# Optimization experiments

Hardware: AMD Instinct MI355X
Metric: run time of the kernel (lower is better)

## Reference

```python
import jax, jax.numpy as jnp
import numpy as np

B, TU, TZ, V, H, E = 64, 128, 16, 32000, 512, 256
EPS = 1e-10


def setup_inputs() -> dict:
    key = jax.random.key(0)
    ks = jax.random.split(key, 22)
    s = 0.02  # weight init scale
    inp = {
        "embed_z": jax.random.normal(ks[0], (1, B, E), jnp.float32),
        "last_hidden": jax.random.normal(ks[1], (1, B, H), jnp.float32),
        "u_enc_out": jax.random.normal(ks[2], (TU, B, H), jnp.float32),
        # previous-turn z posterior: rows are probability distributions over vocab
        "pv_pz_proba": jax.nn.softmax(jax.random.normal(ks[3], (TZ, B, V), jnp.float32), axis=-1),
        "pv_z_dec_out": jax.random.normal(ks[4], (TZ, B, H), jnp.float32),
        "rand_eps": jax.random.normal(ks[5], (B, E), jnp.float32),
        "u_input_np": jax.random.randint(ks[6], (TU, B), 0, V),
        "u_input": jax.random.randint(ks[6], (TU, B), 0, V),   # unused by forward
        "m_input_np": jax.random.randint(ks[7], (TU, B), 0, V),  # unused by forward
        # GRU (single layer, single step)
        "W_ih": jax.random.normal(ks[8], (3 * H, E), jnp.float32) * s,
        "W_hh": jax.random.normal(ks[9], (3 * H, H), jnp.float32) * s,
        "b_ih": jnp.zeros((3 * H,), jnp.float32),
        "b_hh": jnp.zeros((3 * H,), jnp.float32),
        # w1: hidden -> vocab
        "W_w1": jax.random.normal(ks[10], (V, H), jnp.float32) * s,
        "b_w1": jnp.zeros((V,), jnp.float32),
        # proj_copy1 / proj_copy2: hidden -> hidden
        "W_p1": jax.random.normal(ks[11], (H, H), jnp.float32) * s,
        "b_p1": jnp.zeros((H,), jnp.float32),
        "W_p2": jax.random.normal(ks[12], (H, H), jnp.float32) * s,
        "b_p2": jnp.zeros((H,), jnp.float32),
        # mu / log_sigma: vocab -> embed
        "W_mu": jax.random.normal(ks[13], (E, V), jnp.float32) * s,
        "b_mu": jnp.zeros((E,), jnp.float32),
        "W_ls": jax.random.normal(ks[14], (E, V), jnp.float32) * s,
        "b_ls": jnp.zeros((E,), jnp.float32),
    }
    return inp


def reference(embed_z, last_hidden, u_enc_out, pv_pz_proba, pv_z_dec_out, rand_eps,
              u_input_np, u_input, m_input_np,
              W_ih, W_hh, b_ih, b_hh, W_w1, b_w1, W_p1, b_p1, W_p2, b_p2,
              W_mu, b_mu, W_ls, b_ls):
    # --- single GRU step (dropout is identity at rate 0 / eval) ---
    x = embed_z[0]          # (B,E)
    h0 = last_hidden[0]     # (B,H)
    gi = x @ W_ih.T + b_ih
    gh = h0 @ W_hh.T + b_hh
    i_r, i_z, i_n = jnp.split(gi, 3, axis=1)
    h_r, h_z, h_n = jnp.split(gh, 3, axis=1)
    r = jax.nn.sigmoid(i_r + h_r)
    z = jax.nn.sigmoid(i_z + h_z)
    n = jnp.tanh(i_n + r * h_n)
    h = (1.0 - z) * n + z * h0              # (B,H) == gru_out.squeeze(0)

    gen_score = h @ W_w1.T + b_w1           # (B,V)

    # --- user copy score (force_stable path): stable exp + scatter-add by token id ---
    uc = jnp.tanh(jnp.swapaxes(u_enc_out, 0, 1) @ W_p1.T + b_p1)   # (B,TU,H)
    us = jnp.einsum('bth,bh->bt', uc, h)                            # (B,TU)
    um = jnp.max(us, axis=1, keepdims=True)
    ue = jnp.exp(us - um)
    tok = u_input_np.T                                              # (B,TU)
    # sparse one-hot bmm == 1e-10 * sum_t e  +  scatter-add of e into vocab bin tok (tok!=0)
    scat = jnp.zeros((B, V), us.dtype).at[jnp.arange(B)[:, None], tok].add(
        ue * (tok != 0))
    u_copy = jnp.log(EPS * jnp.sum(ue, axis=1, keepdims=True) + scat) + um  # (B,V)

    # --- previous-z copy score (exp path taken when force_stable) ---
    # shift: drop last step, prepend 1e-10 fill
    shifted = jnp.concatenate(
        [jnp.full((1, B, V), EPS, pv_pz_proba.dtype), pv_pz_proba[:-1]], axis=0)  # (TZ,B,V)
    pc = jnp.tanh(jnp.swapaxes(pv_z_dec_out, 0, 1) @ W_p2.T + b_p2)  # (B,TZ,H)
    ps = jnp.exp(jnp.einsum('bth,bh->bt', pc, h))                    # (B,TZ)
    pv_copy = jnp.log(jnp.einsum('bt,tbv->bv', ps, shifted))         # (B,V)

    # --- joint softmax over [gen | u_copy | pv_copy], then merge ---
    scores = jax.nn.softmax(jnp.concatenate([gen_score, u_copy, pv_copy], axis=1), axis=1)
    g, u, p = jnp.split(scores, 3, axis=1)
    proba = g + u + p                        # (B,V)

    # --- VAE reparameterization ---
    appr_emb = proba @ W_mu.T + b_mu         # (B,E)
    log_sigma_ae = proba @ W_ls.T + b_ls
    sampled_ae = appr_emb + jnp.exp(log_sigma_ae) * rand_eps
    return sampled_ae, h[None], h[None], proba, appr_emb, log_sigma_ae
```

## Files before the change

### kernel.cpp

```cpp
#include <hip/hip_runtime.h>
#include <math.h>

#define B 64
#define TU 128
#define TZ 16
#define V 32000
#define H 512
#define E 256
#define EPSC 1e-10f
#define KMZ 125

typedef __attribute__((ext_vector_type(8))) short bf16x8;
typedef __attribute__((ext_vector_type(4))) float f32x4;
#define MFMA16(a, b, c) __builtin_amdgcn_mfma_f32_16x16x32_bf16((a), (b), (c), 0, 0, 0)

union U8 { uint4 u; bf16x8 b; };

__device__ __forceinline__ unsigned short f2bf(float f) {
  unsigned u = __float_as_uint(f);
  u += 0x7FFFu + ((u >> 16) & 1u);
  return (unsigned short)(u >> 16);
}
__device__ __forceinline__ unsigned pack2(float a, float b) {
  return (unsigned)f2bf(a) | ((unsigned)f2bf(b) << 16);
}

__device__ __forceinline__ void stage64x512(unsigned short* __restrict__ dst,
                                            const unsigned short* __restrict__ src)
{
  const int tid = threadIdx.x;
#pragma unroll
  for (int j = 0; j < 16; ++j) {
    const int f = j * 256 + tid;
    const int s = f * 8;
    const int row = s >> 9, col = s & 511;
    *(uint4*)&dst[row * 520 + col] = *(const uint4*)&src[s];
  }
}

__device__ __forceinline__ void stage64x512_f32(unsigned short* __restrict__ dst,
                                                const float* __restrict__ src)
{
  const int tid = threadIdx.x;
#pragma unroll
  for (int j = 0; j < 16; ++j) {
    const int f = j * 256 + tid;
    const int s = f * 8;
    const int row = s >> 9, col = s & 511;
    float4 a = *(const float4*)&src[s];
    float4 b = *(const float4*)&src[s + 4];
    uint4 o;
    o.x = pack2(a.x, a.y); o.y = pack2(a.z, a.w);
    o.z = pack2(b.x, b.y); o.w = pack2(b.z, b.w);
    *(uint4*)&dst[row * 520 + col] = o;
  }
}

__device__ void gemm64_body(const float* __restrict__ A, int lda,
                            const float* __restrict__ Bm, int ldb,
                            const float* __restrict__ bias,
                            float* __restrict__ C, int ldc,
                            int iters, int nb)
{
  __shared__ float As[64][33];
  __shared__ float Bs[64][33];
  const int tid = threadIdx.x;
  const int n0 = nb * 64;
  const int tv = tid & 15, tb = tid >> 4;
  const int lr = tid >> 3;
  const int lc = (tid & 7) << 2;
  float acc[4][4] = {};

  for (int it = 0; it < iters; ++it) {
    const int kb = it * 32;
    float4 a0 = *(const float4*)&A[(size_t)lr * lda + kb + lc];
    float4 a1 = *(const float4*)&A[(size_t)(lr + 32) * lda + kb + lc];
    float4 b0 = *(const float4*)&Bm[(size_t)(n0 + lr) * ldb + kb + lc];
    float4 b1 = *(const float4*)&Bm[(size_t)(n0 + lr + 32) * ldb + kb + lc];
    __syncthreads();
    As[lr][lc] = a0.x; As[lr][lc + 1] = a0.y; As[lr][lc + 2] = a0.z; As[lr][lc + 3] = a0.w;
    As[lr + 32][lc] = a1.x; As[lr + 32][lc + 1] = a1.y; As[lr + 32][lc + 2] = a1.z; As[lr + 32][lc + 3] = a1.w;
    Bs[lr][lc] = b0.x; Bs[lr][lc + 1] = b0.y; Bs[lr][lc + 2] = b0.z; Bs[lr][lc + 3] = b0.w;
    Bs[lr + 32][lc] = b1.x; Bs[lr + 32][lc + 1] = b1.y; Bs[lr + 32][lc + 2] = b1.z; Bs[lr + 32][lc + 3] = b1.w;
    __syncthreads();
#pragma unroll
    for (int kk = 0; kk < 32; ++kk) {
      float av[4], bv[4];
#pragma unroll
      for (int i = 0; i < 4; ++i) av[i] = As[tb * 4 + i][kk];
#pragma unroll
      for (int j = 0; j < 4; ++j) bv[j] = Bs[tv * 4 + j][kk];
#pragma unroll
      for (int i = 0; i < 4; ++i)
#pragma unroll
        for (int j = 0; j < 4; ++j) acc[i][j] += av[i] * bv[j];
    }
  }
#pragma unroll
  for (int i = 0; i < 4; ++i)
#pragma unroll
    for (int j = 0; j < 4; ++j) {
      const int n = n0 + tv * 4 + j;
      C[(size_t)(tb * 4 + i) * ldc + n] = acc[i][j] + bias[n];
    }
}

__global__ __launch_bounds__(256) void k1_prep(
    float* __restrict__ zbuf,
    const float* __restrict__ embed_z, const float* __restrict__ W_ih,
    const float* __restrict__ b_ih, float* __restrict__ gi,
    const float* __restrict__ last_hid, const float* __restrict__ W_hh,
    const float* __restrict__ b_hh, float* __restrict__ gh)
{
  const int bx = blockIdx.x;
  if (bx == 0) {
    for (int i = threadIdx.x; i < 9280; i += 256) zbuf[i] = 0.f;
  } else if (bx < 25) {
    gemm64_body(embed_z, E, W_ih, E, b_ih, gi, 1536, 8, bx - 1);
  } else {
    gemm64_body(last_hid, H, W_hh, H, b_hh, gh, 1536, 16, bx - 25);
  }
}

__global__ void gru_gates(const float* __restrict__ gi, const float* __restrict__ gh,
                          const float* __restrict__ h0, float* __restrict__ h,
                          float* __restrict__ oh1, float* __restrict__ oh2,
                          unsigned short* __restrict__ hbf)
{
  const int b = blockIdx.x, k = threadIdx.x;
  const float ir = gi[b * 1536 + k], iz = gi[b * 1536 + 512 + k], in_ = gi[b * 1536 + 1024 + k];
  const float hr = gh[b * 1536 + k], hz = gh[b * 1536 + 512 + k], hn = gh[b * 1536 + 1024 + k];
  const float r = 1.f / (1.f + __expf(-(ir + hr)));
  const float z = 1.f / (1.f + __expf(-(iz + hz)));
  const float n = tanhf(in_ + r * hn);
  const float hv = (1.f - z) * n + z * h0[b * H + k];
  h[b * H + k] = hv;
  oh1[b * H + k] = hv;
  oh2[b * H + k] = hv;
  hbf[b * H + k] = f2bf(hv);
}

__device__ void us_body_f32(unsigned short* __restrict__ Ws,
                            const float* __restrict__ A,
                            const float* __restrict__ Wm,
                            const float* __restrict__ bias,
                            const float* __restrict__ hvec,
                            float* __restrict__ outp, int T, int m0, int n0)
{
  stage64x512_f32(Ws, Wm + (size_t)n0 * 512);
  __syncthreads();

  const int tid = threadIdx.x;
  const int wave = tid >> 6, lane = tid & 63;
  const int l15 = lane & 15, l4 = lane >> 4;
  const int mbase = m0 + wave * 32;
  const float* ga = A + (size_t)(mbase + l15) * 512 + l4 * 8;

  f32x4 acc[2][4];
#pragma unroll
  for (int i = 0; i < 2; ++i)
#pragma unroll
    for (int j = 0; j < 4; ++j) acc[i][j] = (f32x4)0.f;

#pragma unroll
  for (int it = 0; it < 16; ++it) {
    bf16x8 af[2], bf[4];
#pragma unroll
    for (int i = 0; i < 2; ++i) {
      float4 a0 = *(const float4*)(ga + (size_t)i * 16 * 512 + it * 32);
      float4 a1 = *(const float4*)(ga + (size_t)i * 16 * 512 + it * 32 + 4);
      U8 u;
      u.u.x = pack2(a0.x, a0.y); u.u.y = pack2(a0.z, a0.w);
      u.u.z = pack2(a1.x, a1.y); u.u.w = pack2(a1.z, a1.w);
      af[i] = u.b;
    }
#pragma unroll
    for (int j = 0; j < 4; ++j)
      bf[j] = *(const bf16x8*)&Ws[(j * 16 + l15) * 520 + it * 32 + l4 * 8];
#pragma unroll
    for (int i = 0; i < 2; ++i)
#pragma unroll
      for (int j = 0; j < 4; ++j) acc[i][j] = MFMA16(af[i], bf[j], acc[i][j]);
  }

#pragma unroll
  for (int i = 0; i < 2; ++i) {
#pragma unroll
    for (int q = 0; q < 4; ++q) {
      const int r = mbase + i * 16 + l4 * 4 + q;
      const int b = r & 63;
      float sum = 0.f;
#pragma unroll
      for (int j = 0; j < 4; ++j) {
        const int col = n0 + j * 16 + l15;
        const float x = acc[i][j][q] + bias[col];
        const float ex = __expf(2.f * x);
        const float th = 1.f - 2.f / (ex + 1.f);
        sum += th * hvec[b * H + col];
      }
      sum += __shfl_xor(sum, 1);
      sum += __shfl_xor(sum, 2);
      sum += __shfl_xor(sum, 4);
      sum += __shfl_xor(sum, 8);
      if (l15 == 0) atomicAdd(&outp[b * T + (r >> 6)], sum);
    }
  }
}

__global__ __launch_bounds__(256) void k23(
    const unsigned short* __restrict__ h_bf, const float* __restrict__ W_w1,
    const float* __restrict__ b_w1, float* __restrict__ num,
    const float* __restrict__ u_enc, const float* __restrict__ W_p1,
    const float* __restrict__ b_p1,
    const float* __restrict__ pv_zdec, const float* __restrict__ W_p2,
    const float* __restrict__ b_p2,
    const float* __restrict__ h, float* __restrict__ us, float* __restrict__ pcs)
{
  __shared__ unsigned short sh[64 * 520];
  const int bx = blockIdx.x;
  const int tid = threadIdx.x;
  const int wave = tid >> 6, lane = tid & 63;
  const int l15 = lane & 15, l4 = lane >> 4;

  if (bx < 500) {
    const int n0 = bx * 64;
    const int nrow = n0 + (wave << 4) + l15;
    const float* gw = W_w1 + (size_t)nrow * 512 + l4 * 8;

    float4 wv[32];
#pragma unroll
    for (int it = 0; it < 16; ++it) {
      wv[2 * it]     = *(const float4*)(gw + it * 32);
      wv[2 * it + 1] = *(const float4*)(gw + it * 32 + 4);
    }

    stage64x512(sh, h_bf);
    __syncthreads();

    f32x4 acc[4];
#pragma unroll
    for (int i = 0; i < 4; ++i) acc[i] = (f32x4)0.f;

#pragma unroll
    for (int it = 0; it < 16; ++it) {
      U8 u;
      u.u.x = pack2(wv[2 * it].x, wv[2 * it].y);
      u.u.y = pack2(wv[2 * it].z, wv[2 * it].w);
      u.u.z = pack2(wv[2 * it + 1].x, wv[2 * it + 1].y);
      u.u.w = pack2(wv[2 * it + 1].z, wv[2 * it + 1].w);
#pragma unroll
      for (int i = 0; i < 4; ++i) {
        bf16x8 af = *(const bf16x8*)&sh[(i * 16 + l15) * 520 + it * 32 + l4 * 8];
        acc[i] = MFMA16(af, u.b, acc[i]);
      }
    }

    const float bv = b_w1[nrow];
#pragma unroll
    for (int i = 0; i < 4; ++i)
#pragma unroll
      for (int q = 0; q < 4; ++q) {
        const int row = i * 16 + l4 * 4 + q;
        num[(size_t)row * V + nrow] = acc[i][q] + bv;
      }
  } else if (bx < 1012) {
    const int idx = bx - 500;
    const int xcd = idx & 7, loc = idx >> 3;
    const int m0 = (xcd * 8 + (loc & 7)) * 128;
    const int n0 = (loc >> 3) * 64;
    us_body_f32(sh, u_enc, W_p1, b_p1, h, us, TU, m0, n0);
  } else {
    const int idx = bx - 1012;
    const int m0 = (idx & 7) * 128;
    const int n0 = (idx >> 3) * 64;
    us_body_f32(sh, pv_zdec, W_p2, b_p2, h, pcs, TZ, m0, n0);
  }
}

__global__ void smalls_kernel(const float* __restrict__ us, const float* __restrict__ pcs,
                              float* __restrict__ ue, float* __restrict__ ps,
                              float* __restrict__ base, float* __restrict__ Kb)
{
  const int b = blockIdx.x, t = threadIdx.x;
  __shared__ float sm[128];
  __shared__ float sK;
  const float u = us[b * TU + t];
  sm[t] = u; __syncthreads();
  for (int s = 64; s > 0; s >>= 1) {
    if (t < s) sm[t] = fmaxf(sm[t], sm[t + s]);
    __syncthreads();
  }
  if (t == 0) {
    float um = sm[0];
    float pm = -1e30f;
    for (int q = 0; q < TZ; ++q) pm = fmaxf(pm, pcs[b * TZ + q]);
    sK = fmaxf(fmaxf(um, pm), 0.0f);
  }
  __syncthreads();
  const float K = sK;
  const float e = __expf(u - K);
  ue[b * TU + t] = e;
  sm[t] = e; __syncthreads();
  for (int s = 64; s > 0; s >>= 1) {
    if (t < s) sm[t] += sm[t + s];
    __syncthreads();
  }
  if (t < TZ) ps[b * TZ + t] = __expf(pcs[b * TZ + t] - K);
  if (t == 0) {
    Kb[b] = K;
    base[b] = EPSC * sm[0] + EPSC * __expf(pcs[b * TZ + 0] - K);
  }
}

__global__ __launch_bounds__(256) void pv_fuse(
    float* __restrict__ num, const float* __restrict__ pv,
    const float* __restrict__ ps, const float* __restrict__ base,
    const float* __restrict__ Kb, float* __restrict__ Z)
{
  const int b = blockIdx.y;
  const int i4 = blockIdx.x * 256 + threadIdx.x;
  float local = 0.f;
  if (i4 < V / 4) {
    const float K = Kb[b];
    const float bs = base[b];
    float p[15];
#pragma unroll
    for (int t = 0; t < 15; ++t) p[t] = ps[b * TZ + t + 1];
    float4* row = (float4*)&num[(size_t)b * V];
    float4 g = row[i4];
    float4 e;
    e.x = __expf(g.x - K) + bs;
    e.y = __expf(g.y - K) + bs;
    e.z = __expf(g.z - K) + bs;
    e.w = __expf(g.w - K) + bs;
#pragma unroll
    for (int t = 0; t < 15; ++t) {
      const float4 f = ((const float4*)pv)[((size_t)t * B + b) * (V / 4) + i4];
      e.x += p[t] * f.x; e.y += p[t] * f.y; e.z += p[t] * f.z; e.w += p[t] * f.w;
    }
    row[i4] = e;
    local = e.x + e.y + e.z + e.w;
  }
  __shared__ float sm[256];
  sm[threadIdx.x] = local; __syncthreads();
  for (int st = 128; st > 0; st >>= 1) {
    if (threadIdx.x < st) sm[threadIdx.x] += sm[threadIdx.x + st];
    __syncthreads();
  }
  if (threadIdx.x == 0) atomicAdd(&Z[b], sm[0]);
}

__global__ void scatter_kernel(const int* __restrict__ tok, const float* __restrict__ ue,
                               float* __restrict__ num, float* __restrict__ Z)
{
  const int b = blockIdx.x, t = threadIdx.x;
  const int tk = tok[t * 64 + b];
  float e = 0.f;
  if (tk != 0) {
    e = ue[b * TU + t];
    atomicAdd(&num[(size_t)b * V + tk], e);
  }
  __shared__ float sm[128];
  sm[t] = e; __syncthreads();
  for (int s = 64; s > 0; s >>= 1) {
    if (t < s) sm[t] += sm[t + s];
    __syncthreads();
  }
  if (t == 0) Z[b] = Z[b] + sm[0];
}

__global__ __launch_bounds__(256) void norm2(float* __restrict__ num,
                                             const float* __restrict__ Z,
                                             unsigned short* __restrict__ nb)
{
  const int b = blockIdx.y;
  const int i4 = blockIdx.x * 256 + threadIdx.x;
  if (i4 >= V / 4) return;
  const float r = 1.0f / Z[b];
  float4* row = (float4*)&num[(size_t)b * V];
  float4 v = row[i4];
  v.x *= r; v.y *= r; v.z *= r; v.w *= r;
  row[i4] = v;
  ushort4 o;
  o.x = f2bf(v.x); o.y = f2bf(v.y); o.z = f2bf(v.z); o.w = f2bf(v.w);
  ((ushort4*)&nb[(size_t)b * V])[i4] = o;
}

__global__ __launch_bounds__(256) void k_muls(
    const unsigned short* __restrict__ Ab,
    const float* __restrict__ Wmu, const float* __restrict__ Wls,
    float* __restrict__ pmu, float* __restrict__ pls)
{
  const int tid = threadIdx.x;
  const int wave = tid >> 6, lane = tid & 63;
  const int l15 = lane & 15, l4 = lane >> 4;
  const int cg = blockIdx.x;
  const float* gW = blockIdx.y ? Wls : Wmu;
  float* pO = blockIdx.y ? pls : pmu;
  const int kb0 = blockIdx.z * 256;
  const int c0 = cg * 128 + wave * 32;

  const unsigned short* ga = Ab + (size_t)l15 * V + kb0 + l4 * 8;
  const float* gw0 = gW + (size_t)(c0 + l15) * V + kb0 + l4 * 8;
  const float* gw1 = gW + (size_t)(c0 + 16 + l15) * V + kb0 + l4 * 8;

  f32x4 acc[4][2];
#pragma unroll
  for (int i = 0; i < 4; ++i)
#pragma unroll
    for (int j = 0; j < 2; ++j) acc[i][j] = (f32x4)0.f;

#pragma unroll
  for (int it = 0; it < 8; ++it) {
    const int o = it * 32;
    bf16x8 af[4];
#pragma unroll
    for (int i = 0; i < 4; ++i)
      af[i] = *(const bf16x8*)(ga + (size_t)i * 16 * V + o);
    float4 a0 = *(const float4*)(gw0 + o), a1 = *(const float4*)(gw0 + o + 4);
    float4 b0 = *(const float4*)(gw1 + o), b1 = *(const float4*)(gw1 + o + 4);
    U8 u0, u1;
    u0.u.x = pack2(a0.x, a0.y); u0.u.y = pack2(a0.z, a0.w);
    u0.u.z = pack2(a1.x, a1.y); u0.u.w = pack2(a1.z, a1.w);
    u1.u.x = pack2(b0.x, b0.y); u1.u.y = pack2(b0.z, b0.w);
    u1.u.z = pack2(b1.x, b1.y); u1.u.w = pack2(b1.z, b1.w);
#pragma unroll
    for (int i = 0; i < 4; ++i) {
      acc[i][0] = MFMA16(af[i], u0.b, acc[i][0]);
      acc[i][1] = MFMA16(af[i], u1.b, acc[i][1]);
    }
  }
  const int zo = blockIdx.z * (B * E);
#pragma unroll
  for (int i = 0; i < 4; ++i)
#pragma unroll
    for (int j = 0; j < 2; ++j) {
      const int col = c0 + j * 16 + l15;
#pragma unroll
      for (int q = 0; q < 4; ++q) {
        const int row = i * 16 + l4 * 4 + q;
        pO[zo + row * E + col] = acc[i][j][q];
      }
    }
}

__global__ void final2(const float* __restrict__ pmu, const float* __restrict__ pls,
                       const float* __restrict__ bmu, const float* __restrict__ bls,
                       const float* __restrict__ eps_r, float* __restrict__ out)
{
  const int b = blockIdx.x, e = threadIdx.x;
  float smu = 0.f, sls = 0.f;
  for (int z = 0; z < KMZ; ++z) {
    smu += pmu[z * (B * E) + b * E + e];
    sls += pls[z * (B * E) + b * E + e];
  }
  const float ap = smu + bmu[e];
  const float ls = sls + bls[e];
  out[b * E + e] = ap + __expf(ls) * eps_r[b * E + e];
  out[2129920 + b * E + e] = ap;
  out[2146304 + b * E + e] = ls;
}

extern "C" void kernel_launch(void* const* d_in, const int* in_sizes, int n_in,
                              void* d_out_v, int out_size, void* d_ws, size_t ws_size,
                              hipStream_t stream)
{
  (void)in_sizes; (void)n_in; (void)out_size; (void)ws_size;
  const float* embed_z    = (const float*)d_in[0];
  const float* last_hid   = (const float*)d_in[1];
  const float* u_enc      = (const float*)d_in[2];
  const float* pv_pz      = (const float*)d_in[3];
  const float* pv_zdec    = (const float*)d_in[4];
  const float* rand_eps   = (const float*)d_in[5];
  const int*   u_input_np = (const int*)d_in[6];
  const float* W_ih = (const float*)d_in[9];
  const float* W_hh = (const float*)d_in[10];
  const float* b_ih = (const float*)d_in[11];
  const float* b_hh = (const float*)d_in[12];
  const float* W_w1 = (const float*)d_in[13];
  const float* b_w1 = (const float*)d_in[14];
  const float* W_p1 = (const float*)d_in[15];
  const float* b_p1 = (const float*)d_in[16];
  const float* W_p2 = (const float*)d_in[17];
  const float* b_p2 = (const float*)d_in[18];
  const float* W_mu = (const float*)d_in[19];
  const float* b_mu = (const float*)d_in[20];
  const float* W_ls = (const float*)d_in[21];
  const float* b_ls = (const float*)d_in[22];
  float* d_out = (float*)d_out_v;

  float* ws   = (float*)d_ws;
  float* h    = ws;
  float* gi   = ws + 32768;
  float* gh   = ws + 131072;
  float* us   = ws + 229376;
  float* pcs  = ws + 237568;
  float* Z    = ws + 238592;
  float* ue   = ws + 238656;
  float* ps   = ws + 246848;
  float* base = ws + 247872;
  float* Kb   = ws + 247936;
  unsigned short* h_bf   = (unsigned short*)(ws + 248000);
  unsigned short* num_bf = (unsigned short*)(ws + 526528);
  float* pmu = ws + 1550528;
  float* pls = ws + 3598528;

  float* num   = d_out + 81920;
  float* outh1 = d_out + 16384;
  float* outh2 = d_out + 49152;

  k1_prep<<<dim3(49), 256, 0, stream>>>(
      us ,
      embed_z, W_ih, b_ih, gi, last_hid, W_hh, b_hh, gh);

  gru_gates<<<dim3(B), 512, 0, stream>>>(gi, gh, last_hid, h, outh1, outh2, h_bf);

  k23<<<dim3(1076), 256, 0, stream>>>(
      h_bf, W_w1, b_w1, num,
      u_enc, W_p1, b_p1,
      pv_zdec, W_p2, b_p2,
      h, us, pcs);

  smalls_kernel<<<dim3(B), 128, 0, stream>>>(us, pcs, ue, ps, base, Kb);

  pv_fuse<<<dim3(32, B), 256, 0, stream>>>(num, pv_pz, ps, base, Kb, Z);
  scatter_kernel<<<dim3(B), 128, 0, stream>>>(u_input_np, ue, num, Z);
  norm2<<<dim3(32, B), 256, 0, stream>>>(num, Z, num_bf);

  k_muls<<<dim3(2, 2, KMZ), 256, 0, stream>>>(num_bf, W_mu, W_ls, pmu, pls);
  final2<<<dim3(B), 256, 0, stream>>>(pmu, pls, b_mu, b_ls, rand_eps, d_out);
}
```

Baseline: 165.4 us.

## Fuse softmax/scatter/normalize into cooperative kernel and atomically reduce VAE partials

Restructures the post-GEMM pipeline. The pv-weighted sum moves into a second kernel that runs alongside the u_enc projection. The small max/exp stage, the exp-plus-combine, the token scatter (done in LDS), and the normalize/bf16 pass are merged into one cooperative kernel with two grid syncs. k_muls now accumulates partials atomically and a last-block pass computes the final outputs, which removes the separate reduction kernel and the large partial buffers. This cuts launches and global round trips, at the cost of grid-sync overhead, float atomics that make results order-dependent, and a cooperative launch that needs all 1024 blocks resident at once.

```diff
diff --git a/kernel.cpp b/kernel.cpp
--- a/kernel.cpp
+++ b/kernel.cpp
@@ -1,4 +1,5 @@
 #include <hip/hip_runtime.h>
+#include <hip/hip_cooperative_groups.h>
 #include <math.h>
 
 #define B 64
@@ -114,7 +115,7 @@
 {
   const int bx = blockIdx.x;
   if (bx == 0) {
-    for (int i = threadIdx.x; i < 9280; i += 256) zbuf[i] = 0.f;
+    for (int i = threadIdx.x; i < 42112; i += 256) zbuf[i] = 0.f;
   } else if (bx < 25) {
     gemm64_body(embed_z, E, W_ih, E, b_ih, gi, 1536, 8, bx - 1);
   } else {
@@ -207,14 +208,12 @@
   }
 }
 
-__global__ __launch_bounds__(256) void k23(
+__global__ __launch_bounds__(256) void k23a(
     const unsigned short* __restrict__ h_bf, const float* __restrict__ W_w1,
     const float* __restrict__ b_w1, float* __restrict__ num,
-    const float* __restrict__ u_enc, const float* __restrict__ W_p1,
-    const float* __restrict__ b_p1,
     const float* __restrict__ pv_zdec, const float* __restrict__ W_p2,
-    const float* __restrict__ b_p2,
-    const float* __restrict__ h, float* __restrict__ us, float* __restrict__ pcs)
+    const float* __restrict__ b_p2, const float* __restrict__ h,
+    float* __restrict__ pcs)
 {
   __shared__ unsigned short sh[64 * 520];
   const int bx = blockIdx.x;
@@ -263,142 +262,176 @@
         const int row = i * 16 + l4 * 4 + q;
         num[(size_t)row * V + nrow] = acc[i][q] + bv;
       }
-  } else if (bx < 1012) {
+  } else {
     const int idx = bx - 500;
-    const int xcd = idx & 7, loc = idx >> 3;
+    const int m0 = (idx & 7) * 128;
+    const int n0 = (idx >> 3) * 64;
+    us_body_f32(sh, pv_zdec, W_p2, b_p2, h, pcs, TZ, m0, n0);
+  }
+}
+
+__global__ __launch_bounds__(256) void k23b(
+    const float* __restrict__ u_enc, const float* __restrict__ W_p1,
+    const float* __restrict__ b_p1, const float* __restrict__ h,
+    float* __restrict__ us, const float* __restrict__ pv,
+    const float* __restrict__ pcs, float* __restrict__ Pp)
+{
+  __shared__ unsigned short sh[64 * 520];
+  const int bx = blockIdx.x;
+  if (bx < 512) {
+    const int xcd = bx & 7, loc = bx >> 3;
     const int m0 = (xcd * 8 + (loc & 7)) * 128;
     const int n0 = (loc >> 3) * 64;
     us_body_f32(sh, u_enc, W_p1, b_p1, h, us, TU, m0, n0);
   } else {
-    const int idx = bx - 1012;
-    const int m0 = (idx & 7) * 128;
-    const int n0 = (idx >> 3) * 64;
-    us_body_f32(sh, pv_zdec, W_p2, b_p2, h, pcs, TZ, m0, n0);
-  }
-}
-
-__global__ void smalls_kernel(const float* __restrict__ us, const float* __restrict__ pcs,
-                              float* __restrict__ ue, float* __restrict__ ps,
-                              float* __restrict__ base, float* __restrict__ Kb)
-{
-  const int b = blockIdx.x, t = threadIdx.x;
-  __shared__ float sm[128];
-  __shared__ float sK;
-  const float u = us[b * TU + t];
-  sm[t] = u; __syncthreads();
-  for (int s = 64; s > 0; s >>= 1) {
-    if (t < s) sm[t] = fmaxf(sm[t], sm[t + s]);
+    const int idx = bx - 512;
+    const int b = idx >> 4, c = idx & 15;
+    const int tid = threadIdx.x;
+    float Kp = -1e30f;
+#pragma unroll
+    for (int q = 0; q < TZ; ++q) Kp = fmaxf(Kp, pcs[b * TZ + q]);
+    float w[15];
+#pragma unroll
+    for (int s = 0; s < 15; ++s) w[s] = __expf(pcs[b * TZ + s + 1] - Kp);
+    const float4* pv4 = (const float4*)pv;
+    float4* Pp4 = (float4*)&Pp[(size_t)b * V];
+    const int f0 = c * 500;
+#pragma unroll
+    for (int ji = 0; ji < 2; ++ji) {
+      const int i = tid + ji * 256;
+      if (i < 500) {
+        float4 a = {0.f, 0.f, 0.f, 0.f};
+#pragma unroll
+        for (int s = 0; s < 15; ++s) {
+          const float4 f = pv4[(size_t)(s * B + b) * (V / 4) + f0 + i];
+          a.x += w[s] * f.x; a.y += w[s] * f.y;
+          a.z += w[s] * f.z; a.w += w[s] * f.w;
+        }
+        Pp4[f0 + i] = a;
+      }
+    }
+  }
+}
+
+__global__ __launch_bounds__(256, 4) void coop_finale(
+    const float* __restrict__ us, const float* __restrict__ pcs,
+    float* __restrict__ ue, float* __restrict__ base, float* __restrict__ Kb,
+    float* __restrict__ num, const float* __restrict__ Pp,
+    const int* __restrict__ tok, float* __restrict__ Z,
+    unsigned short* __restrict__ nb)
+{
+  __shared__ float elds[2048];
+  __shared__ float red[256];
+  const int bx = blockIdx.x, tid = threadIdx.x;
+
+  if (bx < B) {
+    const int b0 = bx;
+    float u = (tid < TU) ? us[b0 * TU + tid] : -1e30f;
+    red[tid] = u; __syncthreads();
+    for (int s = 128; s > 0; s >>= 1) {
+      if (tid < s) red[tid] = fmaxf(red[tid], red[tid + s]);
+      __syncthreads();
+    }
+    const float um = red[0];
     __syncthreads();
-  }
-  if (t == 0) {
-    float um = sm[0];
-    float pm = -1e30f;
-    for (int q = 0; q < TZ; ++q) pm = fmaxf(pm, pcs[b * TZ + q]);
-    sK = fmaxf(fmaxf(um, pm), 0.0f);
+    float pm0 = -1e30f;
+    for (int q = 0; q < TZ; ++q) pm0 = fmaxf(pm0, pcs[b0 * TZ + q]);
+    const float K0 = fmaxf(fmaxf(um, pm0), 0.f);
+    float e = 0.f;
+    if (tid < TU) { e = __expf(u - K0); ue[b0 * TU + tid] = e; }
+    red[tid] = e; __syncthreads();
+    for (int s = 128; s > 0; s >>= 1) {
+      if (tid < s) red[tid] += red[tid + s];
+      __syncthreads();
+    }
+    if (tid == 0) {
+      Kb[b0] = K0;
+      base[b0] = EPSC * red[0] + EPSC * __expf(pcs[b0 * TZ] - K0);
+    }
+  }
+  cooperative_groups::this_grid().sync();
+
+  const int b = bx >> 4, c = bx & 15;
+  const float K = Kb[b];
+  const float bs = base[b];
+  float pm = -1e30f;
+  for (int q = 0; q < TZ; ++q) pm = fmaxf(pm, pcs[b * TZ + q]);
+  const float cb = __expf(pm - K);
+  float4* nrow = (float4*)&num[(size_t)b * V];
+  const float4* prow = (const float4*)&Pp[(size_t)b * V];
+  const int f0 = c * 500;
+#pragma unroll
+  for (int ji = 0; ji < 2; ++ji) {
+    const int i = tid + ji * 256;
+    if (i < 500) {
+      float4 g = nrow[f0 + i];
+      float4 pp = prow[f0 + i];
+      float4 e;
+      e.x = __expf(g.x - K) + bs + cb * pp.x;
+      e.y = __expf(g.y - K) + bs + cb * pp.y;
+      e.z = __expf(g.z - K) + bs + cb * pp.z;
+      e.w = __expf(g.w - K) + bs + cb * pp.w;
+      ((float4*)elds)[i] = e;
+    }
   }
   __syncthreads();
-  const float K = sK;
-  const float e = __expf(u - K);
-  ue[b * TU + t] = e;
-  sm[t] = e; __syncthreads();
-  for (int s = 64; s > 0; s >>= 1) {
-    if (t < s) sm[t] += sm[t + s];
+  if (tid < TU) {
+    const int tk = tok[tid * B + b];
+    if (tk != 0) {
+      const int lo = c * 2000;
+      if (tk >= lo && tk < lo + 2000) atomicAdd(&elds[tk - lo], ue[b * TU + tid]);
+    }
+  }
+  __syncthreads();
+  float loc = 0.f;
+#pragma unroll
+  for (int ji = 0; ji < 2; ++ji) {
+    const int i = tid + ji * 256;
+    if (i < 500) {
+      float4 e = ((float4*)elds)[i];
+      loc += e.x + e.y + e.z + e.w;
+    }
+  }
+  red[tid] = loc; __syncthreads();
+  for (int s = 128; s > 0; s >>= 1) {
+    if (tid < s) red[tid] += red[tid + s];
     __syncthreads();
   }
-  if (t < TZ) ps[b * TZ + t] = __expf(pcs[b * TZ + t] - K);
-  if (t == 0) {
-    Kb[b] = K;
-    base[b] = EPSC * sm[0] + EPSC * __expf(pcs[b * TZ + 0] - K);
-  }
-}
-
-__global__ __launch_bounds__(256) void pv_fuse(
-    float* __restrict__ num, const float* __restrict__ pv,
-    const float* __restrict__ ps, const float* __restrict__ base,
-    const float* __restrict__ Kb, float* __restrict__ Z)
-{
-  const int b = blockIdx.y;
-  const int i4 = blockIdx.x * 256 + threadIdx.x;
-  float local = 0.f;
-  if (i4 < V / 4) {
-    const float K = Kb[b];
-    const float bs = base[b];
-    float p[15];
-#pragma unroll
-    for (int t = 0; t < 15; ++t) p[t] = ps[b * TZ + t + 1];
-    float4* row = (float4*)&num[(size_t)b * V];
-    float4 g = row[i4];
-    float4 e;
-    e.x = __expf(g.x - K) + bs;
-    e.y = __expf(g.y - K) + bs;
-    e.z = __expf(g.z - K) + bs;
-    e.w = __expf(g.w - K) + bs;
-#pragma unroll
-    for (int t = 0; t < 15; ++t) {
-      const float4 f = ((const float4*)pv)[((size_t)t * B + b) * (V / 4) + i4];
-      e.x += p[t] * f.x; e.y += p[t] * f.y; e.z += p[t] * f.z; e.w += p[t] * f.w;
-    }
-    row[i4] = e;
-    local = e.x + e.y + e.z + e.w;
-  }
-  __shared__ float sm[256];
-  sm[threadIdx.x] = local; __syncthreads();
-  for (int st = 128; st > 0; st >>= 1) {
-    if (threadIdx.x < st) sm[threadIdx.x] += sm[threadIdx.x + st];
-    __syncthreads();
-  }
-  if (threadIdx.x == 0) atomicAdd(&Z[b], sm[0]);
-}
-
-__global__ void scatter_kernel(const int* __restrict__ tok, const float* __restrict__ ue,
-                               float* __restrict__ num, float* __restrict__ Z)
-{
-  const int b = blockIdx.x, t = threadIdx.x;
-  const int tk = tok[t * 64 + b];
-  float e = 0.f;
-  if (tk != 0) {
-    e = ue[b * TU + t];
-    atomicAdd(&num[(size_t)b * V + tk], e);
-  }
-  __shared__ float sm[128];
-  sm[t] = e; __syncthreads();
-  for (int s = 64; s > 0; s >>= 1) {
-    if (t < s) sm[t] += sm[t + s];
-    __syncthreads();
-  }
-  if (t == 0) Z[b] = Z[b] + sm[0];
-}
-
-__global__ __launch_bounds__(256) void norm2(float* __restrict__ num,
-                                             const float* __restrict__ Z,
-                                             unsigned short* __restrict__ nb)
-{
-  const int b = blockIdx.y;
-  const int i4 = blockIdx.x * 256 + threadIdx.x;
-  if (i4 >= V / 4) return;
+  if (tid == 0) atomicAdd(&Z[b], red[0]);
+  cooperative_groups::this_grid().sync();
+
   const float r = 1.0f / Z[b];
-  float4* row = (float4*)&num[(size_t)b * V];
-  float4 v = row[i4];
-  v.x *= r; v.y *= r; v.z *= r; v.w *= r;
-  row[i4] = v;
-  ushort4 o;
-  o.x = f2bf(v.x); o.y = f2bf(v.y); o.z = f2bf(v.z); o.w = f2bf(v.w);
-  ((ushort4*)&nb[(size_t)b * V])[i4] = o;
+  ushort4* brow = (ushort4*)&nb[(size_t)b * V];
+#pragma unroll
+  for (int ji = 0; ji < 2; ++ji) {
+    const int i = tid + ji * 256;
+    if (i < 500) {
+      float4 v = ((float4*)elds)[i];
+      v.x *= r; v.y *= r; v.z *= r; v.w *= r;
+      nrow[f0 + i] = v;
+      ushort4 o;
+      o.x = f2bf(v.x); o.y = f2bf(v.y); o.z = f2bf(v.z); o.w = f2bf(v.w);
+      brow[f0 + i] = o;
+    }
+  }
 }
 
 __global__ __launch_bounds__(256) void k_muls(
     const unsigned short* __restrict__ Ab,
     const float* __restrict__ Wmu, const float* __restrict__ Wls,
-    float* __restrict__ pmu, float* __restrict__ pls)
+    float* __restrict__ pmu, float* __restrict__ pls,
+    int* __restrict__ cnt,
+    const float* __restrict__ bmu, const float* __restrict__ bls,
+    const float* __restrict__ eps_r, float* __restrict__ out)
 {
   const int tid = threadIdx.x;
   const int wave = tid >> 6, lane = tid & 63;
   const int l15 = lane & 15, l4 = lane >> 4;
-  const int cg = blockIdx.x;
+  const int cgx = blockIdx.x;
   const float* gW = blockIdx.y ? Wls : Wmu;
   float* pO = blockIdx.y ? pls : pmu;
   const int kb0 = blockIdx.z * 256;
-  const int c0 = cg * 128 + wave * 32;
+  const int c0 = cgx * 128 + wave * 32;
 
   const unsigned short* ga = Ab + (size_t)l15 * V + kb0 + l4 * 8;
   const float* gw0 = gW + (size_t)(c0 + l15) * V + kb0 + l4 * 8;
@@ -430,7 +463,6 @@
       acc[i][1] = MFMA16(af[i], u1.b, acc[i][1]);
     }
   }
-  const int zo = blockIdx.z * (B * E);
 #pragma unroll
   for (int i = 0; i < 4; ++i)
 #pragma unroll
@@ -439,26 +471,25 @@
 #pragma unroll
       for (int q = 0; q < 4; ++q) {
         const int row = i * 16 + l4 * 4 + q;
-        pO[zo + row * E + col] = acc[i][j][q];
+        atomicAdd(&pO[row * E + col], acc[i][j][q]);
       }
     }
-}
-
-__global__ void final2(const float* __restrict__ pmu, const float* __restrict__ pls,
-                       const float* __restrict__ bmu, const float* __restrict__ bls,
-                       const float* __restrict__ eps_r, float* __restrict__ out)
-{
-  const int b = blockIdx.x, e = threadIdx.x;
-  float smu = 0.f, sls = 0.f;
-  for (int z = 0; z < KMZ; ++z) {
-    smu += pmu[z * (B * E) + b * E + e];
-    sls += pls[z * (B * E) + b * E + e];
-  }
-  const float ap = smu + bmu[e];
-  const float ls = sls + bls[e];
-  out[b * E + e] = ap + __expf(ls) * eps_r[b * E + e];
-  out[2129920 + b * E + e] = ap;
-  out[2146304 + b * E + e] = ls;
+
+  __threadfence();
+  __shared__ int lastf;
+  if (tid == 0) lastf = (atomicAdd(cnt, 1) == 2 * 2 * KMZ - 1);
+  __syncthreads();
+  if (lastf) {
+    __threadfence();
+    const int e = tid;
+    for (int b = 0; b < B; ++b) {
+      const float ap = pmu[b * E + e] + bmu[e];
+      const float ls = pls[b * E + e] + bls[e];
+      out[b * E + e] = ap + __expf(ls) * eps_r[b * E + e];
+      out[2129920 + b * E + e] = ap;
+      out[2146304 + b * E + e] = ls;
+    }
+  }
 }
 
 extern "C" void kernel_launch(void* const* d_in, const int* in_sizes, int n_in,
@@ -496,14 +527,15 @@
   float* us   = ws + 229376;
   float* pcs  = ws + 237568;
   float* Z    = ws + 238592;
-  float* ue   = ws + 238656;
-  float* ps   = ws + 246848;
-  float* base = ws + 247872;
-  float* Kb   = ws + 247936;
-  unsigned short* h_bf   = (unsigned short*)(ws + 248000);
-  unsigned short* num_bf = (unsigned short*)(ws + 526528);
-  float* pmu = ws + 1550528;
-  float* pls = ws + 3598528;
+  float* pmu  = ws + 238656;
+  float* pls  = ws + 255040;
+  int*   cnt  = (int*)(ws + 271424);
+  float* ue   = ws + 271488;
+  float* base = ws + 279680;
+  float* Kb   = ws + 279744;
+  unsigned short* h_bf = (unsigned short*)(ws + 279808);
+  float* Pp   = ws + 296192;
+  unsigned short* num_bf = (unsigned short*)(ws + 2344192);
 
   float* num   = d_out + 81920;
   float* outh1 = d_out + 16384;
@@ -515,18 +547,28 @@
 
   gru_gates<<<dim3(B), 512, 0, stream>>>(gi, gh, last_hid, h, outh1, outh2, h_bf);
 
-  k23<<<dim3(1076), 256, 0, stream>>>(
-      h_bf, W_w1, b_w1, num,
-      u_enc, W_p1, b_p1,
-      pv_zdec, W_p2, b_p2,
-      h, us, pcs);
-
-  smalls_kernel<<<dim3(B), 128, 0, stream>>>(us, pcs, ue, ps, base, Kb);
-
-  pv_fuse<<<dim3(32, B), 256, 0, stream>>>(num, pv_pz, ps, base, Kb, Z);
-  scatter_kernel<<<dim3(B), 128, 0, stream>>>(u_input_np, ue, num, Z);
-  norm2<<<dim3(32, B), 256, 0, stream>>>(num, Z, num_bf);
-
-  k_muls<<<dim3(2, 2, KMZ), 256, 0, stream>>>(num_bf, W_mu, W_ls, pmu, pls);
-  final2<<<dim3(B), 256, 0, stream>>>(pmu, pls, b_mu, b_ls, rand_eps, d_out);
-}
+  k23a<<<dim3(564), 256, 0, stream>>>(
+      h_bf, W_w1, b_w1, num, pv_zdec, W_p2, b_p2, h, pcs);
+
+  k23b<<<dim3(1536), 256, 0, stream>>>(
+      u_enc, W_p1, b_p1, h, us, pv_pz, pcs, Pp);
+
+  {
+    void* cargs[10];
+    cargs[0] = (void*)&us;
+    cargs[1] = (void*)&pcs;
+    cargs[2] = (void*)&ue;
+    cargs[3] = (void*)&base;
+    cargs[4] = (void*)&Kb;
+    cargs[5] = (void*)&num;
+    cargs[6] = (void*)&Pp;
+    cargs[7] = (void*)&u_input_np;
+    cargs[8] = (void*)&Z;
+    cargs[9] = (void*)&num_bf;
+    hipLaunchCooperativeKernel((void*)coop_finale, dim3(1024), dim3(256),
+                               cargs, 0, stream);
+  }
+
+  k_muls<<<dim3(2, 2, KMZ), 256, 0, stream>>>(
+      num_bf, W_mu, W_ls, pmu, pls, cnt, b_mu, b_ls, rand_eps, d_out);
+}
```

After: 424.7 us. 157% more time.
